# Kernel optimization log

Hardware: AMD Instinct MI355X
Metric: run time of the kernel (lower is better)

## Reference

```python
import jax, jax.numpy as jnp
import numpy as np

B, T, C, H = 4, 2048, 1024, 16
DH = C // H  # 64


def setup_inputs() -> dict:
    key = jax.random.key(0)
    k_x, k_qkv, k_proj = jax.random.split(key, 3)
    x = jax.random.normal(k_x, (B, T, C), dtype=jnp.float32)
    # variance-scaling (fan_in) init for linear weights, torch layout [out, in]
    qkv_w = jax.random.normal(k_qkv, (3 * C, C), dtype=jnp.float32) * (1.0 / np.sqrt(C))
    qkv_b = jnp.zeros((3 * C,), dtype=jnp.float32)
    proj_w = jax.random.normal(k_proj, (C, C), dtype=jnp.float32) * (1.0 / np.sqrt(C))
    proj_b = jnp.zeros((C,), dtype=jnp.float32)
    # causal mask, broadcastable to [B, H, T, T]
    mask = jnp.tril(jnp.ones((T, T), dtype=bool))[None, None]
    return {"x": x, "qkv_w": qkv_w, "qkv_b": qkv_b,
            "proj_w": proj_w, "proj_b": proj_b, "mask": mask}


def reference(x, qkv_w, qkv_b, proj_w, proj_b, mask):
    b, t, c = x.shape
    scale = DH ** -0.5
    qkv = (x @ qkv_w.T + qkv_b).reshape(b, t, 3, H, DH)
    qkv = jnp.transpose(qkv, (2, 0, 3, 1, 4))  # [3, B, H, T, DH]
    q, k, v = qkv[0], qkv[1], qkv[2]
    attn = jnp.einsum("bhqd,bhkd->bhqk", q, k) * scale  # [B, H, T, T]
    neg = -jnp.finfo(attn.dtype).max
    attn = jnp.where(mask, attn, neg)
    attn = jax.nn.softmax(attn, axis=-1)
    out = jnp.einsum("bhqk,bhkd->bhqd", attn, v)  # [B, H, T, DH]
    out = jnp.transpose(out, (0, 2, 1, 3)).reshape(b, t, c)
    return out @ proj_w.T + proj_b
```

## Files before the change

kernel.cpp:

```cpp
#include <hip/hip_runtime.h>
#include <hip/hip_bf16.h>
#include <stdint.h>

#define B_ 4
#define T_ 2048
#define C_ 1024
#define H_ 16
#define DH_ 64
#define M_ (B_*T_)
#define NQKV_ (3*C_)
#define K_ C_

typedef __attribute__((ext_vector_type(8))) short short8;
typedef __attribute__((ext_vector_type(4))) float f32x4;
typedef __attribute__((ext_vector_type(4))) unsigned short us4;

union BFC { __hip_bfloat16 h; unsigned short u; };
__device__ inline unsigned short f2b(float f){ BFC c; c.h = __float2bfloat16(f); return c.u; }

__device__ inline void gload_lds16(const void* g, void* l){
  __builtin_amdgcn_global_load_lds(
    (const __attribute__((address_space(1))) void*)(uintptr_t)g,
    (__attribute__((address_space(3))) void*)(uintptr_t)l,
    16, 0, 0);
}

__global__ void cvt_f32_bf16(const float* __restrict__ src,
                             __hip_bfloat16* __restrict__ dst, int n4)
{
  int i = blockIdx.x * blockDim.x + threadIdx.x;
  int stride = gridDim.x * blockDim.x;
  for (; i < n4; i += stride) {
    float4 v = reinterpret_cast<const float4*>(src)[i];
    us4 o;
    o.x = f2b(v.x); o.y = f2b(v.y); o.z = f2b(v.z); o.w = f2b(v.w);
    reinterpret_cast<us4*>(dst)[i] = o;
  }
}

__global__ __launch_bounds__(256) void gemm_bt(
    const __hip_bfloat16* __restrict__ A,
    const __hip_bfloat16* __restrict__ Bw,
    const float* __restrict__ bias,
    int mode, int nbx,
    __hip_bfloat16* __restrict__ qdst,
    __hip_bfloat16* __restrict__ kdst,
    __hip_bfloat16* __restrict__ vdst,
    float* __restrict__ fdst)
{
  __shared__ char a_lds[2][8192];
  __shared__ char b_lds[2][8192];

  const int tid = threadIdx.x;
  const int lane = tid & 63;
  const int w = tid >> 6;
  const int l15 = lane & 15;
  const int lhi = lane >> 4;
  const int wm = w >> 1, wn = w & 1;

  const int nwg = gridDim.x;
  const int q8 = nwg >> 3;
  const int lb = (blockIdx.x & 7) * q8 + (blockIdx.x >> 3);
  const int bx = lb % nbx, by = lb / nbx;
  const int row0 = by * 128;
  const int col0 = bx * 128;

  int srow[2], scol[2];
#pragma unroll
  for (int j = 0; j < 2; ++j) {
    int L = w * 2048 + j * 1024 + lane * 16;
    int r = L >> 6;
    int cb = (L & 63) ^ (((r >> 1) & 3) << 4);
    srow[j] = r;
    scol[j] = cb >> 1;
  }

  const f32x4 zf = {0.f, 0.f, 0.f, 0.f};
  f32x4 acc[4][4];
#pragma unroll
  for (int m = 0; m < 4; ++m)
#pragma unroll
    for (int n = 0; n < 4; ++n) acc[m][n] = zf;

  const short* Ag = (const short*)A;
  const short* Bg = (const short*)Bw;

#define STAGE(kt, buf)                                                          \
  do {                                                                          \
    gload_lds16(Ag + (size_t)(row0 + srow[0]) * K_ + (kt) + scol[0],            \
                &a_lds[buf][w * 2048]);                                         \
    gload_lds16(Ag + (size_t)(row0 + srow[1]) * K_ + (kt) + scol[1],            \
                &a_lds[buf][w * 2048 + 1024]);                                  \
    gload_lds16(Bg + (size_t)(col0 + srow[0]) * K_ + (kt) + scol[0],            \
                &b_lds[buf][w * 2048]);                                         \
    gload_lds16(Bg + (size_t)(col0 + srow[1]) * K_ + (kt) + scol[1],            \
                &b_lds[buf][w * 2048 + 1024]);                                  \
  } while (0)

  STAGE(0, 0);
  __syncthreads();

  const int NKT = K_ / 32;
  for (int ki = 0; ki < NKT; ++ki) {
    const int cur = ki & 1;
    if (ki + 1 < NKT) STAGE((ki + 1) * 32, cur ^ 1);

    short8 af[4], bfr[4];
#pragma unroll
    for (int m = 0; m < 4; ++m) {
      int r = wm * 64 + m * 16 + l15;
      af[m] = *(const short8*)(&a_lds[cur][r * 64 +
                   ((lhi * 16) ^ (((r >> 1) & 3) << 4))]);
    }
#pragma unroll
    for (int n = 0; n < 4; ++n) {
      int r = wn * 64 + n * 16 + l15;
      bfr[n] = *(const short8*)(&b_lds[cur][r * 64 +
                   ((lhi * 16) ^ (((r >> 1) & 3) << 4))]);
    }
#pragma unroll
    for (int m = 0; m < 4; ++m)
#pragma unroll
      for (int n = 0; n < 4; ++n)
        acc[m][n] = __builtin_amdgcn_mfma_f32_16x16x32_bf16(af[m], bfr[n], acc[m][n], 0, 0, 0);

    __syncthreads();
  }
#undef STAGE

  if (mode == 0) {
#pragma unroll
    for (int m = 0; m < 4; ++m) {
#pragma unroll
      for (int r = 0; r < 4; ++r) {
        int grow = row0 + wm * 64 + m * 16 + lhi * 4 + r;
        int b = grow >> 11, tt = grow & 2047;
#pragma unroll
        for (int n = 0; n < 4; ++n) {
          int gcol = col0 + wn * 64 + n * 16 + l15;
          float v = acc[m][n][r] + bias[gcol];
          int sel = gcol >> 10;
          int c1 = gcol & 1023;
          int hh = c1 >> 6, dh = c1 & 63;
          __hip_bfloat16 bv = __float2bfloat16(v);
          if (sel == 0)
            qdst[(((size_t)(b * H_ + hh)) * T_ + tt) * DH_ + dh] = bv;
          else if (sel == 1)
            kdst[(((size_t)(b * H_ + hh)) * T_ + tt) * DH_ + dh] = bv;
          else
            vdst[(((size_t)(b * H_ + hh)) * DH_ + dh) * T_ + tt] = bv;
        }
      }
    }
  } else {
#pragma unroll
    for (int m = 0; m < 4; ++m) {
#pragma unroll
      for (int r = 0; r < 4; ++r) {
        int grow = row0 + wm * 64 + m * 16 + lhi * 4 + r;
#pragma unroll
        for (int n = 0; n < 4; ++n) {
          int gcol = col0 + wn * 64 + n * 16 + l15;
          fdst[(size_t)grow * C_ + gcol] = acc[m][n][r] + bias[gcol];
        }
      }
    }
  }
}

__global__ __launch_bounds__(512, 2) void attn_kernel(
    const __hip_bfloat16* __restrict__ qg,
    const __hip_bfloat16* __restrict__ kg,
    const __hip_bfloat16* __restrict__ vtg,
    __hip_bfloat16* __restrict__ og)
{
  __shared__ char k_lds[2][8192];
  __shared__ char v_lds[2][8192];
  __shared__ char p_lds[8][4096];

  const int tid = threadIdx.x;
  const int lane = tid & 63;
  const int w = tid >> 6;
  const int l15 = lane & 15;
  const int lhi = lane >> 4;
  const int blk = blockIdx.x;
  const int bh = blk & 63;
  const int g = blk >> 6;
  const int qb = (g < 4) ? g : 11 - g;
  const int qr0 = qb * 256 + w * 32;
  const int nt = 4 * (qb + 1);
  const int tmask = qr0 >> 6;

  const char* kpb = (const char*)(kg + (size_t)bh * T_ * DH_);
  const char* vtpb = (const char*)(vtg + (size_t)bh * DH_ * T_);
  const short* qp = (const short*)(qg + (size_t)bh * T_ * DH_);
  char* pwl = p_lds[w];

  const int srow = tid >> 3;
  const int scb = ((tid & 7) << 4) ^ ((srow & 7) << 4);
  const int sdst = tid * 16;

  short8 qf[2][2];
#pragma unroll
  for (int m = 0; m < 2; ++m)
#pragma unroll
    for (int kf = 0; kf < 2; ++kf)
      qf[m][kf] = *(const short8*)(qp + (size_t)(qr0 + m * 16 + l15) * DH_ +
                                   kf * 32 + lhi * 8);

  const f32x4 zf = {0.f, 0.f, 0.f, 0.f};
  f32x4 o[2][4];
  float lsum[2][4];
#pragma unroll
  for (int m = 0; m < 2; ++m) {
#pragma unroll
    for (int n = 0; n < 4; ++n) o[m][n] = zf;
#pragma unroll
    for (int r = 0; r < 4; ++r) lsum[m][r] = 0.f;
  }

  gload_lds16(kpb + (size_t)srow * 128 + scb, &k_lds[0][sdst]);
  gload_lds16(vtpb + (size_t)srow * 4096 + scb, &v_lds[0][sdst]);
  __syncthreads();

  for (int t = 0; t < nt; ++t) {
    const int cur = t & 1;
    if (t + 1 < nt) {
      const int kv1 = (t + 1) * 64;
      gload_lds16(kpb + (size_t)(kv1 + srow) * 128 + scb, &k_lds[cur ^ 1][sdst]);
      gload_lds16(vtpb + (size_t)srow * 4096 + kv1 * 2 + scb, &v_lds[cur ^ 1][sdst]);
    }

    if (t <= tmask) {
      const int kv0 = t * 64;

      short8 kfr[2][4];
#pragma unroll
      for (int kf = 0; kf < 2; ++kf)
#pragma unroll
        for (int n = 0; n < 4; ++n) {
          int kr = n * 16 + l15;
          kfr[kf][n] = *(const short8*)(&k_lds[cur][kr * 128 +
                           ((kf * 64 + lhi * 16) ^ ((kr & 7) << 4))]);
        }

      f32x4 s[2][4];
#pragma unroll
      for (int m = 0; m < 2; ++m)
#pragma unroll
        for (int n = 0; n < 4; ++n) s[m][n] = zf;
#pragma unroll
      for (int kf = 0; kf < 2; ++kf)
#pragma unroll
        for (int n = 0; n < 4; ++n)
#pragma unroll
          for (int m = 0; m < 2; ++m)
            s[m][n] = __builtin_amdgcn_mfma_f32_16x16x32_bf16(qf[m][kf], kfr[kf][n],
                                                              s[m][n], 0, 0, 0);

      short8 vfr[2][4];
#pragma unroll
      for (int kf = 0; kf < 2; ++kf)
#pragma unroll
        for (int n = 0; n < 4; ++n) {
          int vr = n * 16 + l15;
          vfr[kf][n] = *(const short8*)(&v_lds[cur][vr * 128 +
                           ((kf * 64 + lhi * 16) ^ ((vr & 7) << 4))]);
        }

      if (t == tmask) {
#pragma unroll
        for (int m = 0; m < 2; ++m)
#pragma unroll
          for (int n = 0; n < 4; ++n)
#pragma unroll
            for (int r = 0; r < 4; ++r) {
              int kvA = kv0 + n * 16 + l15;
              int qA = qr0 + m * 16 + lhi * 4 + r;
              if (kvA > qA) s[m][n][r] = -1e30f;
            }
      }

#pragma unroll
      for (int m = 0; m < 2; ++m)
#pragma unroll
        for (int n = 0; n < 4; ++n)
#pragma unroll
          for (int r = 0; r < 4; ++r) {
            float pe = __expf(s[m][n][r] * 0.125f);
            s[m][n][r] = pe;
            lsum[m][r] += pe;
          }

#pragma unroll
      for (int m = 0; m < 2; ++m)
#pragma unroll
        for (int n = 0; n < 4; ++n)
#pragma unroll
          for (int r = 0; r < 4; ++r) {
            int row = m * 16 + lhi * 4 + r;
            *(unsigned short*)(pwl + row * 128 +
                               (((n * 16 + l15) * 2) ^ ((row & 7) << 4))) =
                f2b(s[m][n][r]);
          }
      short8 pa[2][2];
#pragma unroll
      for (int m = 0; m < 2; ++m)
#pragma unroll
        for (int kf = 0; kf < 2; ++kf) {
          int row = m * 16 + l15;
          pa[m][kf] = *(const short8*)(pwl + row * 128 +
                                       ((kf * 64 + lhi * 16) ^ ((row & 7) << 4)));
        }

#pragma unroll
      for (int kf = 0; kf < 2; ++kf)
#pragma unroll
        for (int n = 0; n < 4; ++n)
#pragma unroll
          for (int m = 0; m < 2; ++m)
            o[m][n] = __builtin_amdgcn_mfma_f32_16x16x32_bf16(pa[m][kf], vfr[kf][n],
                                                              o[m][n], 0, 0, 0);
    }

    __syncthreads();
  }

#pragma unroll
  for (int m = 0; m < 2; ++m)
#pragma unroll
    for (int r = 0; r < 4; ++r)
#pragma unroll
      for (int d = 1; d < 16; d <<= 1)
        lsum[m][r] += __shfl_xor(lsum[m][r], d, 64);

  const int b = bh >> 4, hd = bh & 15;
#pragma unroll
  for (int m = 0; m < 2; ++m)
#pragma unroll
    for (int r = 0; r < 4; ++r) {
      float inv = 1.f / lsum[m][r];
      int qrow = qr0 + m * 16 + lhi * 4 + r;
      __hip_bfloat16* orow = og + ((size_t)(b * T_ + qrow)) * C_ + hd * DH_;
#pragma unroll
      for (int n = 0; n < 4; ++n)
        orow[n * 16 + l15] = __float2bfloat16(o[m][n][r] * inv);
    }
}

extern "C" void kernel_launch(void* const* d_in, const int* in_sizes, int n_in,
                              void* d_out, int out_size, void* d_ws, size_t ws_size,
                              hipStream_t stream) {
  const float* x      = (const float*)d_in[0];
  const float* qkv_w  = (const float*)d_in[1];
  const float* qkv_b  = (const float*)d_in[2];
  const float* proj_w = (const float*)d_in[3];
  const float* proj_b = (const float*)d_in[4];
  float* out = (float*)d_out;

  char* ws = (char*)d_ws;
  __hip_bfloat16* xb    = (__hip_bfloat16*)(ws);
  __hip_bfloat16* wqkv  = (__hip_bfloat16*)(ws + 16777216);
  __hip_bfloat16* wproj = (__hip_bfloat16*)(ws + 23068672);
  __hip_bfloat16* qb    = (__hip_bfloat16*)(ws + 25165824);
  __hip_bfloat16* kb    = (__hip_bfloat16*)(ws + 41943040);
  __hip_bfloat16* vtb   = (__hip_bfloat16*)(ws + 58720256);
  __hip_bfloat16* att   = (__hip_bfloat16*)(ws + 75497472);

  cvt_f32_bf16<<<2048, 256, 0, stream>>>(x, xb, M_ * K_ / 4);
  cvt_f32_bf16<<<1024, 256, 0, stream>>>(qkv_w, wqkv, NQKV_ * K_ / 4);
  cvt_f32_bf16<<<512, 256, 0, stream>>>(proj_w, wproj, C_ * K_ / 4);

  gemm_bt<<<dim3((NQKV_/128) * (M_/128)), 256, 0, stream>>>(
      xb, wqkv, qkv_b, 0, NQKV_/128, qb, kb, vtb, nullptr);

  attn_kernel<<<dim3(512), 512, 0, stream>>>(qb, kb, vtb, att);

  gemm_bt<<<dim3((C_/128) * (M_/128)), 256, 0, stream>>>(
      att, wproj, proj_b, 1, C_/128, nullptr, nullptr, nullptr, out);
}
```

Measured before the change: 208.8 us.

## Enlarge GEMM tiles to 256x256x64 with 8 waves per block

The GEMM kernel moves from 128x128 tiles with 4 waves and a K-step of 32 to 256x256 tiles with 8 waves and a K-step of 64. The LDS swizzle and staging are redone for 128-byte rows. The goal is to raise arithmetic intensity and reduce global and LDS traffic per MFMA. In exchange it uses 128KB of LDS and more accumulator registers, and it shrinks the grid to 384 and 128 blocks, which may leave CUs idle, especially in the projection GEMM.

New measurement: 200.9 us. 3.8% less time.

```diff
diff --git a/kernel.cpp b/kernel.cpp
--- a/kernel.cpp
+++ b/kernel.cpp
@@ -38,7 +38,7 @@
   }
 }
 
-__global__ __launch_bounds__(256) void gemm_bt(
+__global__ __launch_bounds__(512) void gemm_bt(
     const __hip_bfloat16* __restrict__ A,
     const __hip_bfloat16* __restrict__ Bw,
     const float* __restrict__ bias,
@@ -48,37 +48,37 @@
     __hip_bfloat16* __restrict__ vdst,
     float* __restrict__ fdst)
 {
-  __shared__ char a_lds[2][8192];
-  __shared__ char b_lds[2][8192];
+  __shared__ char a_lds[2][32768];
+  __shared__ char b_lds[2][32768];
 
   const int tid = threadIdx.x;
   const int lane = tid & 63;
   const int w = tid >> 6;
   const int l15 = lane & 15;
   const int lhi = lane >> 4;
-  const int wm = w >> 1, wn = w & 1;
+  const int wm = w >> 2, wn = w & 3;
 
   const int nwg = gridDim.x;
   const int q8 = nwg >> 3;
   const int lb = (blockIdx.x & 7) * q8 + (blockIdx.x >> 3);
   const int bx = lb % nbx, by = lb / nbx;
-  const int row0 = by * 128;
-  const int col0 = bx * 128;
-
-  int srow[2], scol[2];
-#pragma unroll
-  for (int j = 0; j < 2; ++j) {
-    int L = w * 2048 + j * 1024 + lane * 16;
-    int r = L >> 6;
-    int cb = (L & 63) ^ (((r >> 1) & 3) << 4);
-    srow[j] = r;
-    scol[j] = cb >> 1;
+  const int row0 = by * 256;
+  const int col0 = bx * 256;
+
+  int srow[4], scol[4];
+#pragma unroll
+  for (int i = 0; i < 4; ++i) {
+    int L = i * 8192 + tid * 16;
+    int r = L >> 7;
+    int cb = (L & 127) ^ ((r & 7) << 4);
+    srow[i] = r;
+    scol[i] = cb >> 1;
   }
 
   const f32x4 zf = {0.f, 0.f, 0.f, 0.f};
-  f32x4 acc[4][4];
-#pragma unroll
-  for (int m = 0; m < 4; ++m)
+  f32x4 acc[8][4];
+#pragma unroll
+  for (int m = 0; m < 8; ++m)
 #pragma unroll
     for (int n = 0; n < 4; ++n) acc[m][n] = zf;
 
@@ -87,42 +87,45 @@
 
 #define STAGE(kt, buf)                                                          \
   do {                                                                          \
-    gload_lds16(Ag + (size_t)(row0 + srow[0]) * K_ + (kt) + scol[0],            \
-                &a_lds[buf][w * 2048]);                                         \
-    gload_lds16(Ag + (size_t)(row0 + srow[1]) * K_ + (kt) + scol[1],            \
-                &a_lds[buf][w * 2048 + 1024]);                                  \
-    gload_lds16(Bg + (size_t)(col0 + srow[0]) * K_ + (kt) + scol[0],            \
-                &b_lds[buf][w * 2048]);                                         \
-    gload_lds16(Bg + (size_t)(col0 + srow[1]) * K_ + (kt) + scol[1],            \
-                &b_lds[buf][w * 2048 + 1024]);                                  \
+    _Pragma("unroll")                                                           \
+    for (int i = 0; i < 4; ++i) {                                               \
+      gload_lds16(Ag + (size_t)(row0 + srow[i]) * K_ + (kt) + scol[i],          \
+                  &a_lds[buf][i * 8192 + tid * 16]);                            \
+      gload_lds16(Bg + (size_t)(col0 + srow[i]) * K_ + (kt) + scol[i],          \
+                  &b_lds[buf][i * 8192 + tid * 16]);                            \
+    }                                                                           \
   } while (0)
 
   STAGE(0, 0);
   __syncthreads();
 
-  const int NKT = K_ / 32;
+  const int NKT = K_ / 64;
   for (int ki = 0; ki < NKT; ++ki) {
     const int cur = ki & 1;
-    if (ki + 1 < NKT) STAGE((ki + 1) * 32, cur ^ 1);
-
-    short8 af[4], bfr[4];
-#pragma unroll
-    for (int m = 0; m < 4; ++m) {
-      int r = wm * 64 + m * 16 + l15;
-      af[m] = *(const short8*)(&a_lds[cur][r * 64 +
-                   ((lhi * 16) ^ (((r >> 1) & 3) << 4))]);
-    }
-#pragma unroll
-    for (int n = 0; n < 4; ++n) {
-      int r = wn * 64 + n * 16 + l15;
-      bfr[n] = *(const short8*)(&b_lds[cur][r * 64 +
-                   ((lhi * 16) ^ (((r >> 1) & 3) << 4))]);
-    }
-#pragma unroll
-    for (int m = 0; m < 4; ++m)
-#pragma unroll
-      for (int n = 0; n < 4; ++n)
-        acc[m][n] = __builtin_amdgcn_mfma_f32_16x16x32_bf16(af[m], bfr[n], acc[m][n], 0, 0, 0);
+    if (ki + 1 < NKT) STAGE((ki + 1) * 64, cur ^ 1);
+
+#pragma unroll
+    for (int kf = 0; kf < 2; ++kf) {
+      short8 af[8], bfr[4];
+#pragma unroll
+      for (int m = 0; m < 8; ++m) {
+        int r = wm * 128 + m * 16 + l15;
+        af[m] = *(const short8*)(&a_lds[cur][r * 128 +
+                     ((kf * 64 + lhi * 16) ^ ((r & 7) << 4))]);
+      }
+#pragma unroll
+      for (int n = 0; n < 4; ++n) {
+        int r = wn * 64 + n * 16 + l15;
+        bfr[n] = *(const short8*)(&b_lds[cur][r * 128 +
+                     ((kf * 64 + lhi * 16) ^ ((r & 7) << 4))]);
+      }
+#pragma unroll
+      for (int m = 0; m < 8; ++m)
+#pragma unroll
+        for (int n = 0; n < 4; ++n)
+          acc[m][n] = __builtin_amdgcn_mfma_f32_16x16x32_bf16(af[m], bfr[n],
+                                                              acc[m][n], 0, 0, 0);
+    }
 
     __syncthreads();
   }
@@ -130,10 +133,10 @@
 
   if (mode == 0) {
 #pragma unroll
-    for (int m = 0; m < 4; ++m) {
+    for (int m = 0; m < 8; ++m) {
 #pragma unroll
       for (int r = 0; r < 4; ++r) {
-        int grow = row0 + wm * 64 + m * 16 + lhi * 4 + r;
+        int grow = row0 + wm * 128 + m * 16 + lhi * 4 + r;
         int b = grow >> 11, tt = grow & 2047;
 #pragma unroll
         for (int n = 0; n < 4; ++n) {
@@ -154,10 +157,10 @@
     }
   } else {
 #pragma unroll
-    for (int m = 0; m < 4; ++m) {
+    for (int m = 0; m < 8; ++m) {
 #pragma unroll
       for (int r = 0; r < 4; ++r) {
-        int grow = row0 + wm * 64 + m * 16 + lhi * 4 + r;
+        int grow = row0 + wm * 128 + m * 16 + lhi * 4 + r;
 #pragma unroll
         for (int n = 0; n < 4; ++n) {
           int gcol = col0 + wn * 64 + n * 16 + l15;
@@ -371,11 +374,11 @@
   cvt_f32_bf16<<<1024, 256, 0, stream>>>(qkv_w, wqkv, NQKV_ * K_ / 4);
   cvt_f32_bf16<<<512, 256, 0, stream>>>(proj_w, wproj, C_ * K_ / 4);
 
-  gemm_bt<<<dim3((NQKV_/128) * (M_/128)), 256, 0, stream>>>(
-      xb, wqkv, qkv_b, 0, NQKV_/128, qb, kb, vtb, nullptr);
+  gemm_bt<<<dim3((NQKV_/256) * (M_/256)), 512, 0, stream>>>(
+      xb, wqkv, qkv_b, 0, NQKV_/256, qb, kb, vtb, nullptr);
 
   attn_kernel<<<dim3(512), 512, 0, stream>>>(qb, kb, vtb, att);
 
-  gemm_bt<<<dim3((C_/128) * (M_/128)), 256, 0, stream>>>(
-      att, wproj, proj_b, 1, C_/128, nullptr, nullptr, nullptr, out);
-}
+  gemm_bt<<<dim3((C_/256) * (M_/256)), 512, 0, stream>>>(
+      att, wproj, proj_b, 1, C_/256, nullptr, nullptr, nullptr, out);
+}
```

## Enlarge GEMM tiles to 256x256 with 16 waves and MFMA priority boost

Applied to the files above, without the earlier changes.

The GEMM kernel moves from 128x128 tiles with 4 waves to 256x256 tiles with 16 waves per block. LDS staging is redone with a new row-pair XOR swizzle, and each thread now issues one 16-byte load per operand per k-step. The MFMA block is wrapped in s_setprio so waves doing math get issue priority over those loading. Bigger tiles cut global traffic per FLOP, but they also mean fewer blocks (for example 128 for the output projection), which risks under-filling the CUs, and 32KB of LDS per double-buffered operand.

After: 205.0 us. About the same (-1.8%).

```diff
diff --git a/kernel.cpp b/kernel.cpp
--- a/kernel.cpp
+++ b/kernel.cpp
@@ -38,7 +38,7 @@
   }
 }
 
-__global__ __launch_bounds__(256) void gemm_bt(
+__global__ __launch_bounds__(1024) void gemm_bt(
     const __hip_bfloat16* __restrict__ A,
     const __hip_bfloat16* __restrict__ Bw,
     const float* __restrict__ bias,
@@ -48,32 +48,28 @@
     __hip_bfloat16* __restrict__ vdst,
     float* __restrict__ fdst)
 {
-  __shared__ char a_lds[2][8192];
-  __shared__ char b_lds[2][8192];
+  __shared__ char a_lds[2][16384];
+  __shared__ char b_lds[2][16384];
 
   const int tid = threadIdx.x;
   const int lane = tid & 63;
   const int w = tid >> 6;
   const int l15 = lane & 15;
   const int lhi = lane >> 4;
-  const int wm = w >> 1, wn = w & 1;
+  const int wm = w >> 2, wn = w & 3;
 
   const int nwg = gridDim.x;
   const int q8 = nwg >> 3;
   const int lb = (blockIdx.x & 7) * q8 + (blockIdx.x >> 3);
   const int bx = lb % nbx, by = lb / nbx;
-  const int row0 = by * 128;
-  const int col0 = bx * 128;
-
-  int srow[2], scol[2];
-#pragma unroll
-  for (int j = 0; j < 2; ++j) {
-    int L = w * 2048 + j * 1024 + lane * 16;
-    int r = L >> 6;
-    int cb = (L & 63) ^ (((r >> 1) & 3) << 4);
-    srow[j] = r;
-    scol[j] = cb >> 1;
-  }
+  const int row0 = by * 256;
+  const int col0 = bx * 256;
+
+  const int s_ = tid >> 3;
+  const int oo = ((tid & 7) << 4) ^ ((s_ & 7) << 4);
+  const int srow = 2 * s_ + ((oo >> 6) & 1);
+  const int scol = ((oo >> 4) & 3) * 8;
+  const int sdst = tid * 16;
 
   const f32x4 zf = {0.f, 0.f, 0.f, 0.f};
   f32x4 acc[4][4];
@@ -85,44 +81,46 @@
   const short* Ag = (const short*)A;
   const short* Bg = (const short*)Bw;
 
-#define STAGE(kt, buf)                                                          \
-  do {                                                                          \
-    gload_lds16(Ag + (size_t)(row0 + srow[0]) * K_ + (kt) + scol[0],            \
-                &a_lds[buf][w * 2048]);                                         \
-    gload_lds16(Ag + (size_t)(row0 + srow[1]) * K_ + (kt) + scol[1],            \
-                &a_lds[buf][w * 2048 + 1024]);                                  \
-    gload_lds16(Bg + (size_t)(col0 + srow[0]) * K_ + (kt) + scol[0],            \
-                &b_lds[buf][w * 2048]);                                         \
-    gload_lds16(Bg + (size_t)(col0 + srow[1]) * K_ + (kt) + scol[1],            \
-                &b_lds[buf][w * 2048 + 1024]);                                  \
+#define STAGE(kt, buf)                                                         \
+  do {                                                                         \
+    gload_lds16(Ag + (size_t)(row0 + srow) * K_ + (kt) * 32 + scol,            \
+                &a_lds[buf][sdst]);                                            \
+    gload_lds16(Bg + (size_t)(col0 + srow) * K_ + (kt) * 32 + scol,            \
+                &b_lds[buf][sdst]);                                            \
   } while (0)
 
   STAGE(0, 0);
   __syncthreads();
 
   const int NKT = K_ / 32;
-  for (int ki = 0; ki < NKT; ++ki) {
-    const int cur = ki & 1;
-    if (ki + 1 < NKT) STAGE((ki + 1) * 32, cur ^ 1);
+  for (int t = 0; t < NKT; ++t) {
+    const int cur = t & 1;
+    if (t + 1 < NKT) STAGE(t + 1, cur ^ 1);
 
     short8 af[4], bfr[4];
 #pragma unroll
     for (int m = 0; m < 4; ++m) {
       int r = wm * 64 + m * 16 + l15;
-      af[m] = *(const short8*)(&a_lds[cur][r * 64 +
-                   ((lhi * 16) ^ (((r >> 1) & 3) << 4))]);
+      int addr = (r >> 1) * 128 +
+                 ((((r & 1) << 6) | (lhi << 4)) ^ (((r >> 1) & 7) << 4));
+      af[m] = *(const short8*)(&a_lds[cur][addr]);
     }
 #pragma unroll
     for (int n = 0; n < 4; ++n) {
       int r = wn * 64 + n * 16 + l15;
-      bfr[n] = *(const short8*)(&b_lds[cur][r * 64 +
-                   ((lhi * 16) ^ (((r >> 1) & 3) << 4))]);
-    }
+      int addr = (r >> 1) * 128 +
+                 ((((r & 1) << 6) | (lhi << 4)) ^ (((r >> 1) & 7) << 4));
+      bfr[n] = *(const short8*)(&b_lds[cur][addr]);
+    }
+
+    __builtin_amdgcn_s_setprio(1);
 #pragma unroll
     for (int m = 0; m < 4; ++m)
 #pragma unroll
       for (int n = 0; n < 4; ++n)
-        acc[m][n] = __builtin_amdgcn_mfma_f32_16x16x32_bf16(af[m], bfr[n], acc[m][n], 0, 0, 0);
+        acc[m][n] = __builtin_amdgcn_mfma_f32_16x16x32_bf16(af[m], bfr[n],
+                                                            acc[m][n], 0, 0, 0);
+    __builtin_amdgcn_s_setprio(0);
 
     __syncthreads();
   }
@@ -371,11 +369,11 @@
   cvt_f32_bf16<<<1024, 256, 0, stream>>>(qkv_w, wqkv, NQKV_ * K_ / 4);
   cvt_f32_bf16<<<512, 256, 0, stream>>>(proj_w, wproj, C_ * K_ / 4);
 
-  gemm_bt<<<dim3((NQKV_/128) * (M_/128)), 256, 0, stream>>>(
-      xb, wqkv, qkv_b, 0, NQKV_/128, qb, kb, vtb, nullptr);
+  gemm_bt<<<dim3((NQKV_/256) * (M_/256)), 1024, 0, stream>>>(
+      xb, wqkv, qkv_b, 0, NQKV_/256, qb, kb, vtb, nullptr);
 
   attn_kernel<<<dim3(512), 512, 0, stream>>>(qb, kb, vtb, att);
 
-  gemm_bt<<<dim3((C_/128) * (M_/128)), 256, 0, stream>>>(
-      att, wproj, proj_b, 1, C_/128, nullptr, nullptr, nullptr, out);
-}
+  gemm_bt<<<dim3((C_/256) * (M_/256)), 1024, 0, stream>>>(
+      att, wproj, proj_b, 1, C_/256, nullptr, nullptr, nullptr, out);
+}
```
